# Kernel tuning notes

Measured on AMD Instinct MI355X. Metric: run time of the kernel, lower is better.

Reference implementation:

```python
import jax, jax.numpy as jnp
import numpy as np

B, L, D, H = 4, 1024, 1024, 16
DK = D // H


def setup_inputs() -> dict:
    key = jax.random.key(0)
    ks = jax.random.split(key, 5)
    s = 1.0 / np.sqrt(D)  # roughly nn.Linear init scale
    return {
        "x": jax.random.normal(ks[0], (B, L, D), dtype=jnp.float32),
        "Wq": jax.random.normal(ks[1], (D, D), dtype=jnp.float32) * s,
        "bq": jnp.zeros((D,), dtype=jnp.float32),
        "Wk": jax.random.normal(ks[2], (D, D), dtype=jnp.float32) * s,
        "bk": jnp.zeros((D,), dtype=jnp.float32),
        "Wv": jax.random.normal(ks[3], (D, D), dtype=jnp.float32) * s,
        "bv": jnp.zeros((D,), dtype=jnp.float32),
        "Wo": jax.random.normal(ks[4], (D, D), dtype=jnp.float32) * s,
        "bo": jnp.zeros((D,), dtype=jnp.float32),
    }


def reference(x, Wq, bq, Wk, bk, Wv, bv, Wo, bo):
    b, l, d = x.shape
    # torch Linear: y = x @ W.T + b
    q = (x @ Wq.T + bq).reshape(b, l, H, DK).transpose(0, 2, 1, 3)  # [B,H,L,DK]
    k = (x @ Wk.T + bk).reshape(b, l, H, DK).transpose(0, 2, 1, 3)
    v = (x @ Wv.T + bv).reshape(b, l, H, DK).transpose(0, 2, 1, 3)
    scores = jnp.einsum("bhqd,bhkd->bhqk", q, k) / jnp.sqrt(jnp.float32(DK))
    attn = jax.nn.softmax(scores, axis=-1)  # dropout p=0 -> identity
    head_out = jnp.einsum("bhqk,bhkd->bhqd", attn, v)  # [B,H,L,DK]
    merged = head_out.transpose(0, 2, 1, 3).reshape(b, l, d)  # [B,L,D]
    out = merged @ Wo.T + bo
    # DeCov loss over head outputs
    U = merged.reshape(b * l, d)
    U = U - U.mean(axis=0, keepdims=True)
    C = (U.T @ U) / jnp.float32(b * l)
    decov = 0.5 * (jnp.sum(C * C) - jnp.sum(jnp.diag(C) ** 2))
    return (out, decov)
```

## Files before the change

kernel.cpp:

```cpp
#include <hip/hip_runtime.h>
#include <cstdint>
#include <cstddef>

typedef short v4s __attribute__((ext_vector_type(4)));
typedef short v8s __attribute__((ext_vector_type(8)));
typedef float v4f __attribute__((ext_vector_type(4)));

__device__ __forceinline__ short f2bf(float f) {
    union { float f; unsigned u; } x; x.f = f;
    unsigned r = (x.u + 0x7FFFu + ((x.u >> 16) & 1u)) >> 16;
    return (short)(unsigned short)r;
}
__device__ __forceinline__ float bf2f(short h) {
    union { unsigned u; float f; } x; x.u = ((unsigned)(unsigned short)h) << 16;
    return x.f;
}

__device__ __forceinline__ void gld16(const void* g, void* l) {
    __builtin_amdgcn_global_load_lds((const __attribute__((address_space(1))) void*)g,
                                     (__attribute__((address_space(3))) void*)l, 16, 0, 0);
}

__global__ __launch_bounds__(256) void cvt_bf16(
    const float* __restrict__ x, const float* __restrict__ wq, const float* __restrict__ wk,
    const float* __restrict__ wv, const float* __restrict__ wo,
    short* __restrict__ xb, short* __restrict__ wqb, short* __restrict__ wkb,
    short* __restrict__ wvb, short* __restrict__ wob)
{
    int bid = blockIdx.x;
    const float* src; short* dst; size_t base;
    if (bid < 4096)      { src = x;  dst = xb;  base = (size_t)bid * 1024; }
    else if (bid < 5120) { src = wq; dst = wqb; base = (size_t)(bid - 4096) * 1024; }
    else if (bid < 6144) { src = wk; dst = wkb; base = (size_t)(bid - 5120) * 1024; }
    else if (bid < 7168) { src = wv; dst = wvb; base = (size_t)(bid - 6144) * 1024; }
    else                 { src = wo; dst = wob; base = (size_t)(bid - 7168) * 1024; }
    size_t idx = base + (size_t)threadIdx.x * 4;
    v4f v = *(const v4f*)(src + idx);
    v4s o;
    o[0] = f2bf(v[0]); o[1] = f2bf(v[1]); o[2] = f2bf(v[2]); o[3] = f2bf(v[3]);
    *(v4s*)(dst + idx) = o;
}

__global__ __launch_bounds__(256) void gemm_qkv(
    const short* __restrict__ xb,
    const short* __restrict__ wq, const short* __restrict__ wk, const short* __restrict__ wv,
    const float* __restrict__ bq, const float* __restrict__ bk, const float* __restrict__ bv,
    short* __restrict__ qo, short* __restrict__ ko, short* __restrict__ vto)
{
    __shared__ __align__(16) short At[128 * 32];
    __shared__ __align__(16) short Bt[128 * 32];
    const int K = 1024;
    const int mode = blockIdx.z;
    const short* W = (mode == 0) ? wq : (mode == 1) ? wk : wv;
    const float* bias = (mode == 0) ? bq : (mode == 1) ? bk : bv;
    const int m0 = blockIdx.y * 128, n0 = blockIdx.x * 128;
    const int tid = threadIdx.x, wave = tid >> 6, lane = tid & 63;
    const int quad = lane >> 4, ll = lane & 15;
    const int wr = wave >> 1, wc = wave & 1;
    const v4f zero4 = {0.f, 0.f, 0.f, 0.f};
    v4f acc[4][4];
    for (int i = 0; i < 4; ++i) for (int j = 0; j < 4; ++j) acc[i][j] = zero4;

    for (int k0 = 0; k0 < K; k0 += 32) {
        __syncthreads();
#pragma unroll
        for (int c = 0; c < 2; ++c) {
            int chb = (wave * 2 + c) * 64;
            int ch = chb + lane;
            int row = ch >> 2, col8 = (ch & 3) * 8;
            gld16(xb + (size_t)(m0 + row) * K + k0 + col8, &At[chb * 8]);
            gld16(W  + (size_t)(n0 + row) * K + k0 + col8, &Bt[chb * 8]);
        }
        __syncthreads();
        v8s af[4], bfr[4];
#pragma unroll
        for (int i = 0; i < 4; ++i) af[i]  = *(const v8s*)&At[(wr * 64 + i * 16 + ll) * 32 + quad * 8];
#pragma unroll
        for (int j = 0; j < 4; ++j) bfr[j] = *(const v8s*)&Bt[(wc * 64 + j * 16 + ll) * 32 + quad * 8];
#pragma unroll
        for (int i = 0; i < 4; ++i)
#pragma unroll
            for (int j = 0; j < 4; ++j)
                acc[i][j] = __builtin_amdgcn_mfma_f32_16x16x32_bf16(af[i], bfr[j], acc[i][j], 0, 0, 0);
    }

    const float scale = (mode == 0) ? 0.125f : 1.0f;
#pragma unroll
    for (int j = 0; j < 4; ++j) {
        int n = n0 + wc * 64 + j * 16 + ll;
        float bb = bias[n];
        int hh = n >> 6, dk = n & 63;
#pragma unroll
        for (int i = 0; i < 4; ++i) {
            int mbase = m0 + wr * 64 + i * 16 + quad * 4;
#pragma unroll
            for (int r = 0; r < 4; ++r) {
                int m = mbase + r;
                int b = m >> 10, li = m & 1023;
                short h = f2bf((acc[i][j][r] + bb) * scale);
                if (mode == 0)
                    qo[(((size_t)(b * 16 + hh) * 1024 + li) << 6) + dk] = h;
                else if (mode == 1)
                    ko[(((size_t)(b * 16 + hh) * 1024 + li) << 6) + dk] = h;
                else
                    vto[(((size_t)(b * 16 + hh) * 64 + dk) << 10) + li] = h;
            }
        }
    }
}

__global__ __launch_bounds__(256) void gemm_out(
    const short* __restrict__ A, const short* __restrict__ W,
    const float* __restrict__ bias, float* __restrict__ out)
{
    __shared__ __align__(16) short At[128 * 32];
    __shared__ __align__(16) short Bt[128 * 32];
    const int K = 1024;
    const int m0 = blockIdx.y * 128, n0 = blockIdx.x * 128;
    const int tid = threadIdx.x, wave = tid >> 6, lane = tid & 63;
    const int quad = lane >> 4, ll = lane & 15;
    const int wr = wave >> 1, wc = wave & 1;
    const v4f zero4 = {0.f, 0.f, 0.f, 0.f};
    v4f acc[4][4];
    for (int i = 0; i < 4; ++i) for (int j = 0; j < 4; ++j) acc[i][j] = zero4;

    for (int k0 = 0; k0 < K; k0 += 32) {
        __syncthreads();
#pragma unroll
        for (int c = 0; c < 2; ++c) {
            int chb = (wave * 2 + c) * 64;
            int ch = chb + lane;
            int row = ch >> 2, col8 = (ch & 3) * 8;
            gld16(A + (size_t)(m0 + row) * K + k0 + col8, &At[chb * 8]);
            gld16(W + (size_t)(n0 + row) * K + k0 + col8, &Bt[chb * 8]);
        }
        __syncthreads();
        v8s af[4], bfr[4];
#pragma unroll
        for (int i = 0; i < 4; ++i) af[i]  = *(const v8s*)&At[(wr * 64 + i * 16 + ll) * 32 + quad * 8];
#pragma unroll
        for (int j = 0; j < 4; ++j) bfr[j] = *(const v8s*)&Bt[(wc * 64 + j * 16 + ll) * 32 + quad * 8];
#pragma unroll
        for (int i = 0; i < 4; ++i)
#pragma unroll
            for (int j = 0; j < 4; ++j)
                acc[i][j] = __builtin_amdgcn_mfma_f32_16x16x32_bf16(af[i], bfr[j], acc[i][j], 0, 0, 0);
    }

#pragma unroll
    for (int j = 0; j < 4; ++j) {
        int n = n0 + wc * 64 + j * 16 + ll;
        float bb = bias[n];
#pragma unroll
        for (int i = 0; i < 4; ++i) {
            int mbase = m0 + wr * 64 + i * 16 + quad * 4;
#pragma unroll
            for (int r = 0; r < 4; ++r) {
                int m = mbase + r;
                out[(size_t)m * 1024 + n] = acc[i][j][r] + bb;
            }
        }
    }
}

__global__ __launch_bounds__(256) void attn_flash(
    const short* __restrict__ qb, const short* __restrict__ kb, const short* __restrict__ vtb,
    float* __restrict__ merged, short* __restrict__ mergedh)
{
    __shared__ __align__(16) short Kt[64 * 64];
    __shared__ __align__(16) short Vt[64 * 64];
    __shared__ __align__(16) short Pt[4 * 16 * 68];
    const int bh = blockIdx.y, qt = blockIdx.x;
    const int tid = threadIdx.x, wave = tid >> 6, lane = tid & 63;
    const int quad = lane >> 4, ll = lane & 15;
    const short* qp = qb  + (size_t)bh * 1024 * 64;
    const short* kp = kb  + (size_t)bh * 1024 * 64;
    const short* vp = vtb + (size_t)bh * 64 * 1024;

    const int qrow = qt * 64 + wave * 16 + ll;
    v8s qa0 = *(const v8s*)(qp + (size_t)qrow * 64 + quad * 8);
    v8s qa1 = *(const v8s*)(qp + (size_t)qrow * 64 + 32 + quad * 8);

    const v4f zero4 = {0.f, 0.f, 0.f, 0.f};
    v4f oacc[4];
    for (int nt = 0; nt < 4; ++nt) oacc[nt] = zero4;
    float lsum[4] = {0.f, 0.f, 0.f, 0.f};
    short* pw = &Pt[wave * 16 * 68];

    for (int jt = 0; jt < 16; ++jt) {
        __syncthreads();
#pragma unroll
        for (int c = 0; c < 2; ++c) {
            int chb = (wave * 2 + c) * 64;
            int ch = chb + lane;
            int row = ch >> 3;
            int gi = ((ch & 7) ^ (row & 7)) * 8;
            gld16(kp + (size_t)(jt * 64 + row) * 64 + gi, &Kt[chb * 8]);
            gld16(vp + (size_t)row * 1024 + jt * 64 + gi, &Vt[chb * 8]);
        }
        __syncthreads();

        v4f sacc[4];
#pragma unroll
        for (int nt = 0; nt < 4; ++nt) {
            int n = nt * 16 + ll;
            int g0 = (quad ^ (n & 7)) * 8;
            int g1 = ((4 + quad) ^ (n & 7)) * 8;
            v8s b0 = *(const v8s*)&Kt[n * 64 + g0];
            v8s b1 = *(const v8s*)&Kt[n * 64 + g1];
            v4f s = zero4;
            s = __builtin_amdgcn_mfma_f32_16x16x32_bf16(qa0, b0, s, 0, 0, 0);
            s = __builtin_amdgcn_mfma_f32_16x16x32_bf16(qa1, b1, s, 0, 0, 0);
            sacc[nt] = s;
        }
#pragma unroll
        for (int nt = 0; nt < 4; ++nt) {
#pragma unroll
            for (int r = 0; r < 4; ++r) {
                float e = __expf(sacc[nt][r]);
                lsum[r] += e;
                pw[(quad * 4 + r) * 68 + nt * 16 + ll] = f2bf(e);
            }
        }
        __syncthreads();
        v4s p00 = *(const v4s*)&pw[ll * 68 + quad * 8];
        v4s p01 = *(const v4s*)&pw[ll * 68 + quad * 8 + 4];
        v4s p10 = *(const v4s*)&pw[ll * 68 + 32 + quad * 8];
        v4s p11 = *(const v4s*)&pw[ll * 68 + 32 + quad * 8 + 4];
        v8s pa0 = __builtin_shufflevector(p00, p01, 0, 1, 2, 3, 4, 5, 6, 7);
        v8s pa1 = __builtin_shufflevector(p10, p11, 0, 1, 2, 3, 4, 5, 6, 7);
#pragma unroll
        for (int nt = 0; nt < 4; ++nt) {
            int n = nt * 16 + ll;
            int g0 = (quad ^ (n & 7)) * 8;
            int g1 = ((4 + quad) ^ (n & 7)) * 8;
            v8s v0 = *(const v8s*)&Vt[n * 64 + g0];
            v8s v1 = *(const v8s*)&Vt[n * 64 + g1];
            oacc[nt] = __builtin_amdgcn_mfma_f32_16x16x32_bf16(pa0, v0, oacc[nt], 0, 0, 0);
            oacc[nt] = __builtin_amdgcn_mfma_f32_16x16x32_bf16(pa1, v1, oacc[nt], 0, 0, 0);
        }
    }

    float linv[4];
#pragma unroll
    for (int r = 0; r < 4; ++r) {
        float s = lsum[r];
        s += __shfl_xor(s, 1); s += __shfl_xor(s, 2);
        s += __shfl_xor(s, 4); s += __shfl_xor(s, 8);
        linv[r] = 1.0f / s;
    }
    const int b = bh >> 4, h = bh & 15;
#pragma unroll
    for (int r = 0; r < 4; ++r) {
        int li = qt * 64 + wave * 16 + quad * 4 + r;
        size_t rowoff = ((size_t)(b * 1024 + li)) * 1024 + h * 64;
#pragma unroll
        for (int nt = 0; nt < 4; ++nt) {
            int d = nt * 16 + ll;
            float v = oacc[nt][r] * linv[r];
            merged[rowoff + d] = v;
            mergedh[rowoff + d] = f2bf(v);
        }
    }
}

__global__ __launch_bounds__(256) void col_part(const float* __restrict__ merged, float* __restrict__ part) {
    const int bi = blockIdx.x, t = threadIdx.x;
    const float* base = merged + (size_t)bi * 32 * 1024 + (size_t)t * 4;
    float s0 = 0.f, s1 = 0.f, s2 = 0.f, s3 = 0.f;
    for (int r = 0; r < 32; ++r) {
        v4f v = *(const v4f*)(base + (size_t)r * 1024);
        s0 += v[0]; s1 += v[1]; s2 += v[2]; s3 += v[3];
    }
    v4f o = {s0, s1, s2, s3};
    *(v4f*)(part + (size_t)bi * 1024 + (size_t)t * 4) = o;
}

__global__ __launch_bounds__(256) void col_mean(const float* __restrict__ part, float* __restrict__ mean) {
    int c = blockIdx.x * 256 + threadIdx.x;
    float s = 0.f;
    for (int i = 0; i < 128; ++i) s += part[i * 1024 + c];
    mean[c] = s * (1.0f / 4096.0f);
}

__global__ __launch_bounds__(256) void center_tr(
    const float* __restrict__ merged, const float* __restrict__ cmean,
    short* __restrict__ uth, short* __restrict__ utl)
{
    __shared__ short Hh[64][72];
    __shared__ short Hl[64][72];
    const int d0 = blockIdx.x * 64, m0 = blockIdx.y * 64;
    const int t = threadIdx.x;
    const int r0 = t >> 4, c4 = (t & 15) * 4;
    float mu[4];
#pragma unroll
    for (int e = 0; e < 4; ++e) mu[e] = cmean[d0 + c4 + e];
    for (int rr = 0; rr < 64; rr += 16) {
        int m = m0 + rr + r0;
        v4f v = *(const v4f*)(merged + (size_t)m * 1024 + d0 + c4);
#pragma unroll
        for (int e = 0; e < 4; ++e) {
            float u = v[e] - mu[e];
            short h = f2bf(u);
            Hh[c4 + e][rr + r0] = h;
            Hl[c4 + e][rr + r0] = f2bf(u - bf2f(h));
        }
    }
    __syncthreads();
    const int d = t >> 2, mg = (t & 3) * 16;
    v8s a0, a1, b0, b1;
#pragma unroll
    for (int e = 0; e < 8; ++e) {
        a0[e] = Hh[d][mg + e]; a1[e] = Hh[d][mg + 8 + e];
        b0[e] = Hl[d][mg + e]; b1[e] = Hl[d][mg + 8 + e];
    }
    size_t off = (size_t)(d0 + d) * 4096 + m0 + mg;
    *(v8s*)(uth + off) = a0; *(v8s*)(uth + off + 8) = a1;
    *(v8s*)(utl + off) = b0; *(v8s*)(utl + off + 8) = b1;
}

__global__ __launch_bounds__(256) void gemm_decov(
    const short* __restrict__ uth, const short* __restrict__ utl, float* __restrict__ cpart)
{
    int p = blockIdx.x, I = 0, rem = p;
    while (rem >= 16 - I) { rem -= 16 - I; ++I; }
    const int J = I + rem;
    const int kbase = blockIdx.y * 512;
    __shared__ __align__(16) short Ah[64 * 32], Al[64 * 32], Bh[64 * 32], Bl[64 * 32];
    const int tid = threadIdx.x;
    const int wave = tid >> 6, lane = tid & 63;
    const int quad = lane >> 4, ll = lane & 15;
    const int wr = wave >> 1, wc = wave & 1;
    const v4f zero4 = {0.f, 0.f, 0.f, 0.f};
    v4f acc[2][2];
    for (int i = 0; i < 2; ++i) for (int j = 0; j < 2; ++j) acc[i][j] = zero4;

    for (int kk = 0; kk < 512; kk += 32) {
        int k0 = kbase + kk;
        __syncthreads();
        {
            int ch = wave * 64 + lane;
            int row = ch >> 2, col8 = (ch & 3) * 8;
            gld16(uth + (size_t)(I * 64 + row) * 4096 + k0 + col8, &Ah[wave * 512]);
            gld16(utl + (size_t)(I * 64 + row) * 4096 + k0 + col8, &Al[wave * 512]);
            gld16(uth + (size_t)(J * 64 + row) * 4096 + k0 + col8, &Bh[wave * 512]);
            gld16(utl + (size_t)(J * 64 + row) * 4096 + k0 + col8, &Bl[wave * 512]);
        }
        __syncthreads();
        v8s ah[2], al[2], bh[2], bl[2];
#pragma unroll
        for (int i = 0; i < 2; ++i) {
            int ro = (wr * 32 + i * 16 + ll) * 32 + quad * 8;
            ah[i] = *(const v8s*)&Ah[ro];
            al[i] = *(const v8s*)&Al[ro];
        }
#pragma unroll
        for (int j = 0; j < 2; ++j) {
            int ro = (wc * 32 + j * 16 + ll) * 32 + quad * 8;
            bh[j] = *(const v8s*)&Bh[ro];
            bl[j] = *(const v8s*)&Bl[ro];
        }
#pragma unroll
        for (int i = 0; i < 2; ++i)
#pragma unroll
            for (int j = 0; j < 2; ++j) {
                acc[i][j] = __builtin_amdgcn_mfma_f32_16x16x32_bf16(ah[i], bh[j], acc[i][j], 0, 0, 0);
                acc[i][j] = __builtin_amdgcn_mfma_f32_16x16x32_bf16(ah[i], bl[j], acc[i][j], 0, 0, 0);
                acc[i][j] = __builtin_amdgcn_mfma_f32_16x16x32_bf16(al[i], bh[j], acc[i][j], 0, 0, 0);
            }
    }

    float* dst = cpart + ((size_t)blockIdx.y * 136 + p) * 4096;
#pragma unroll
    for (int i = 0; i < 2; ++i)
#pragma unroll
        for (int j = 0; j < 2; ++j)
#pragma unroll
            for (int r = 0; r < 4; ++r) {
                int gi2 = wr * 32 + i * 16 + quad * 4 + r;
                int gj2 = wc * 32 + j * 16 + ll;
                dst[gi2 * 64 + gj2] = acc[i][j][r];
            }
}

__global__ __launch_bounds__(256) void decov_reduce(const float* __restrict__ cpart, float* __restrict__ dsum) {
    int p = blockIdx.x, I = 0, rem = p;
    while (rem >= 16 - I) { rem -= 16 - I; ++I; }
    const int J = I + rem;
    const int t = threadIdx.x;
    __shared__ float wsums[4];
    float s = 0.f;
    for (int e = t; e < 4096; e += 256) {
        float c = 0.f;
#pragma unroll
        for (int kc = 0; kc < 8; ++kc) c += cpart[((size_t)kc * 136 + p) * 4096 + e];
        int gi = I * 64 + (e >> 6), gj = J * 64 + (e & 63);
        if (gi != gj) s += c * c;
    }
    if (I < J) s *= 2.f;
    s += __shfl_xor(s, 1); s += __shfl_xor(s, 2); s += __shfl_xor(s, 4);
    s += __shfl_xor(s, 8); s += __shfl_xor(s, 16); s += __shfl_xor(s, 32);
    if ((t & 63) == 0) wsums[t >> 6] = s;
    __syncthreads();
    if (t == 0) dsum[p] = wsums[0] + wsums[1] + wsums[2] + wsums[3];
}

__global__ __launch_bounds__(256) void decov_final(const float* __restrict__ dsum, float* __restrict__ out) {
    const int t = threadIdx.x;
    __shared__ float wsums[4];
    float s = (t < 136) ? dsum[t] : 0.f;
    s += __shfl_xor(s, 1); s += __shfl_xor(s, 2); s += __shfl_xor(s, 4);
    s += __shfl_xor(s, 8); s += __shfl_xor(s, 16); s += __shfl_xor(s, 32);
    if ((t & 63) == 0) wsums[t >> 6] = s;
    __syncthreads();
    if (t == 0) {
        float tot = wsums[0] + wsums[1] + wsums[2] + wsums[3];
        out[4194304] = 0.5f * tot / (4096.0f * 4096.0f);
    }
}

extern "C" void kernel_launch(void* const* d_in, const int* in_sizes, int n_in,
                              void* d_out, int out_size, void* d_ws, size_t ws_size,
                              hipStream_t stream) {
    const float* x  = (const float*)d_in[0];
    const float* Wq = (const float*)d_in[1];
    const float* bq = (const float*)d_in[2];
    const float* Wk = (const float*)d_in[3];
    const float* bk = (const float*)d_in[4];
    const float* Wv = (const float*)d_in[5];
    const float* bv = (const float*)d_in[6];
    const float* Wo = (const float*)d_in[7];
    const float* bo = (const float*)d_in[8];
    float* out = (float*)d_out;
    char* ws = (char*)d_ws;
    const size_t MB = 1ull << 20;
    short* xb      = (short*)(ws);
    short* wqb     = (short*)(ws + 8  * MB);
    short* wkb     = (short*)(ws + 10 * MB);
    short* wvb     = (short*)(ws + 12 * MB);
    short* wob     = (short*)(ws + 14 * MB);
    short* qb      = (short*)(ws + 16 * MB);
    short* kb      = (short*)(ws + 24 * MB);
    short* vtb     = (short*)(ws + 32 * MB);
    float* merged  = (float*)(ws + 40 * MB);
    short* mergedh = (short*)(ws + 56 * MB);
    float* colpart = (float*)(ws + 64 * MB);
    float* colmean = (float*)(ws + 64 * MB + 512 * 1024);
    short* uth     = (short*)(ws + 65 * MB);
    short* utl     = (short*)(ws + 73 * MB);
    float* dsum    = (float*)(ws + 81 * MB);
    float* cpart   = (float*)(ws);

    hipLaunchKernelGGL(cvt_bf16, dim3(8192), dim3(256), 0, stream,
                       x, Wq, Wk, Wv, Wo, xb, wqb, wkb, wvb, wob);
    hipLaunchKernelGGL(gemm_qkv, dim3(8, 32, 3), dim3(256), 0, stream,
                       xb, wqb, wkb, wvb, bq, bk, bv, qb, kb, vtb);
    hipLaunchKernelGGL(attn_flash, dim3(16, 64), dim3(256), 0, stream,
                       qb, kb, vtb, merged, mergedh);
    hipLaunchKernelGGL(gemm_out, dim3(8, 32), dim3(256), 0, stream,
                       mergedh, wob, bo, out);
    hipLaunchKernelGGL(col_part, dim3(128), dim3(256), 0, stream, merged, colpart);
    hipLaunchKernelGGL(col_mean, dim3(4), dim3(256), 0, stream, colpart, colmean);
    hipLaunchKernelGGL(center_tr, dim3(16, 64), dim3(256), 0, stream,
                       merged, colmean, uth, utl);
    hipLaunchKernelGGL(gemm_decov, dim3(136, 8), dim3(256), 0, stream, uth, utl, cpart);
    hipLaunchKernelGGL(decov_reduce, dim3(136), dim3(256), 0, stream, cpart, dsum);
    hipLaunchKernelGGL(decov_final, dim3(1), dim3(256), 0, stream, dsum, out);
}
```

Before: 252.3 us.

## Double GEMM K-tile with XOR-swizzled LDS and give attention waves 32 query rows

The three MFMA GEMM kernels (QKV projection, output projection, DeCov covariance) now stage 64-wide K tiles instead of 32. They use an XOR-swizzled LDS layout, which halves the number of barriers per K and is meant to avoid bank conflicts on the fragment reads. The flash attention kernel now gives each wave 32 query rows instead of 16 and launches half as many blocks. Each K/V tile loaded into LDS is therefore reused across twice as many queries. The trade-off is higher register and LDS use, fewer blocks, and lower occupancy.

```diff
diff --git a/kernel.cpp b/kernel.cpp
--- a/kernel.cpp
+++ b/kernel.cpp
@@ -47,8 +47,8 @@
     const float* __restrict__ bq, const float* __restrict__ bk, const float* __restrict__ bv,
     short* __restrict__ qo, short* __restrict__ ko, short* __restrict__ vto)
 {
-    __shared__ __align__(16) short At[128 * 32];
-    __shared__ __align__(16) short Bt[128 * 32];
+    __shared__ __align__(16) short At[128 * 64];
+    __shared__ __align__(16) short Bt[128 * 64];
     const int K = 1024;
     const int mode = blockIdx.z;
     const short* W = (mode == 0) ? wq : (mode == 1) ? wk : wv;
@@ -61,27 +61,33 @@
     v4f acc[4][4];
     for (int i = 0; i < 4; ++i) for (int j = 0; j < 4; ++j) acc[i][j] = zero4;
 
-    for (int k0 = 0; k0 < K; k0 += 32) {
-        __syncthreads();
-#pragma unroll
-        for (int c = 0; c < 2; ++c) {
-            int chb = (wave * 2 + c) * 64;
-            int ch = chb + lane;
-            int row = ch >> 2, col8 = (ch & 3) * 8;
-            gld16(xb + (size_t)(m0 + row) * K + k0 + col8, &At[chb * 8]);
-            gld16(W  + (size_t)(n0 + row) * K + k0 + col8, &Bt[chb * 8]);
-        }
-        __syncthreads();
-        v8s af[4], bfr[4];
-#pragma unroll
-        for (int i = 0; i < 4; ++i) af[i]  = *(const v8s*)&At[(wr * 64 + i * 16 + ll) * 32 + quad * 8];
-#pragma unroll
-        for (int j = 0; j < 4; ++j) bfr[j] = *(const v8s*)&Bt[(wc * 64 + j * 16 + ll) * 32 + quad * 8];
-#pragma unroll
-        for (int i = 0; i < 4; ++i)
-#pragma unroll
-            for (int j = 0; j < 4; ++j)
-                acc[i][j] = __builtin_amdgcn_mfma_f32_16x16x32_bf16(af[i], bfr[j], acc[i][j], 0, 0, 0);
+    const int srow = (lane >> 3);
+    const int sgi = ((lane & 7) ^ srow) * 8;
+
+    for (int k0 = 0; k0 < K; k0 += 64) {
+        __syncthreads();
+#pragma unroll
+        for (int c = 0; c < 4; ++c) {
+            int g = wave * 4 + c;
+            int row = g * 8 + srow;
+            gld16(xb + (size_t)(m0 + row) * K + k0 + sgi, &At[g * 512]);
+            gld16(W  + (size_t)(n0 + row) * K + k0 + sgi, &Bt[g * 512]);
+        }
+        __syncthreads();
+#pragma unroll
+        for (int s = 0; s < 2; ++s) {
+            const int xo = ((s * 4 + quad) ^ (ll & 7)) * 8;
+            v8s af[4], bfr[4];
+#pragma unroll
+            for (int i = 0; i < 4; ++i) af[i]  = *(const v8s*)&At[(wr * 64 + i * 16 + ll) * 64 + xo];
+#pragma unroll
+            for (int j = 0; j < 4; ++j) bfr[j] = *(const v8s*)&Bt[(wc * 64 + j * 16 + ll) * 64 + xo];
+#pragma unroll
+            for (int i = 0; i < 4; ++i)
+#pragma unroll
+                for (int j = 0; j < 4; ++j)
+                    acc[i][j] = __builtin_amdgcn_mfma_f32_16x16x32_bf16(af[i], bfr[j], acc[i][j], 0, 0, 0);
+        }
     }
 
     const float scale = (mode == 0) ? 0.125f : 1.0f;
@@ -113,8 +119,8 @@
     const short* __restrict__ A, const short* __restrict__ W,
     const float* __restrict__ bias, float* __restrict__ out)
 {
-    __shared__ __align__(16) short At[128 * 32];
-    __shared__ __align__(16) short Bt[128 * 32];
+    __shared__ __align__(16) short At[128 * 64];
+    __shared__ __align__(16) short Bt[128 * 64];
     const int K = 1024;
     const int m0 = blockIdx.y * 128, n0 = blockIdx.x * 128;
     const int tid = threadIdx.x, wave = tid >> 6, lane = tid & 63;
@@ -124,27 +130,33 @@
     v4f acc[4][4];
     for (int i = 0; i < 4; ++i) for (int j = 0; j < 4; ++j) acc[i][j] = zero4;
 
-    for (int k0 = 0; k0 < K; k0 += 32) {
-        __syncthreads();
-#pragma unroll
-        for (int c = 0; c < 2; ++c) {
-            int chb = (wave * 2 + c) * 64;
-            int ch = chb + lane;
-            int row = ch >> 2, col8 = (ch & 3) * 8;
-            gld16(A + (size_t)(m0 + row) * K + k0 + col8, &At[chb * 8]);
-            gld16(W + (size_t)(n0 + row) * K + k0 + col8, &Bt[chb * 8]);
-        }
-        __syncthreads();
-        v8s af[4], bfr[4];
-#pragma unroll
-        for (int i = 0; i < 4; ++i) af[i]  = *(const v8s*)&At[(wr * 64 + i * 16 + ll) * 32 + quad * 8];
-#pragma unroll
-        for (int j = 0; j < 4; ++j) bfr[j] = *(const v8s*)&Bt[(wc * 64 + j * 16 + ll) * 32 + quad * 8];
-#pragma unroll
-        for (int i = 0; i < 4; ++i)
-#pragma unroll
-            for (int j = 0; j < 4; ++j)
-                acc[i][j] = __builtin_amdgcn_mfma_f32_16x16x32_bf16(af[i], bfr[j], acc[i][j], 0, 0, 0);
+    const int srow = (lane >> 3);
+    const int sgi = ((lane & 7) ^ srow) * 8;
+
+    for (int k0 = 0; k0 < K; k0 += 64) {
+        __syncthreads();
+#pragma unroll
+        for (int c = 0; c < 4; ++c) {
+            int g = wave * 4 + c;
+            int row = g * 8 + srow;
+            gld16(A + (size_t)(m0 + row) * K + k0 + sgi, &At[g * 512]);
+            gld16(W + (size_t)(n0 + row) * K + k0 + sgi, &Bt[g * 512]);
+        }
+        __syncthreads();
+#pragma unroll
+        for (int s = 0; s < 2; ++s) {
+            const int xo = ((s * 4 + quad) ^ (ll & 7)) * 8;
+            v8s af[4], bfr[4];
+#pragma unroll
+            for (int i = 0; i < 4; ++i) af[i]  = *(const v8s*)&At[(wr * 64 + i * 16 + ll) * 64 + xo];
+#pragma unroll
+            for (int j = 0; j < 4; ++j) bfr[j] = *(const v8s*)&Bt[(wc * 64 + j * 16 + ll) * 64 + xo];
+#pragma unroll
+            for (int i = 0; i < 4; ++i)
+#pragma unroll
+                for (int j = 0; j < 4; ++j)
+                    acc[i][j] = __builtin_amdgcn_mfma_f32_16x16x32_bf16(af[i], bfr[j], acc[i][j], 0, 0, 0);
+        }
     }
 
 #pragma unroll
@@ -169,7 +181,7 @@
 {
     __shared__ __align__(16) short Kt[64 * 64];
     __shared__ __align__(16) short Vt[64 * 64];
-    __shared__ __align__(16) short Pt[4 * 16 * 68];
+    __shared__ __align__(16) short Pt[4 * 32 * 68];
     const int bh = blockIdx.y, qt = blockIdx.x;
     const int tid = threadIdx.x, wave = tid >> 6, lane = tid & 63;
     const int quad = lane >> 4, ll = lane & 15;
@@ -177,15 +189,20 @@
     const short* kp = kb  + (size_t)bh * 1024 * 64;
     const short* vp = vtb + (size_t)bh * 64 * 1024;
 
-    const int qrow = qt * 64 + wave * 16 + ll;
-    v8s qa0 = *(const v8s*)(qp + (size_t)qrow * 64 + quad * 8);
-    v8s qa1 = *(const v8s*)(qp + (size_t)qrow * 64 + 32 + quad * 8);
+    v8s qa[2][2];
+#pragma unroll
+    for (int mi = 0; mi < 2; ++mi) {
+        int qrow = qt * 128 + wave * 32 + mi * 16 + ll;
+        qa[mi][0] = *(const v8s*)(qp + (size_t)qrow * 64 + quad * 8);
+        qa[mi][1] = *(const v8s*)(qp + (size_t)qrow * 64 + 32 + quad * 8);
+    }
 
     const v4f zero4 = {0.f, 0.f, 0.f, 0.f};
-    v4f oacc[4];
-    for (int nt = 0; nt < 4; ++nt) oacc[nt] = zero4;
-    float lsum[4] = {0.f, 0.f, 0.f, 0.f};
-    short* pw = &Pt[wave * 16 * 68];
+    v4f oacc[2][4];
+    for (int mi = 0; mi < 2; ++mi) for (int nt = 0; nt < 4; ++nt) oacc[mi][nt] = zero4;
+    float lsum[2][4];
+    for (int mi = 0; mi < 2; ++mi) for (int r = 0; r < 4; ++r) lsum[mi][r] = 0.f;
+    short* pw = &Pt[wave * 32 * 68];
 
     for (int jt = 0; jt < 16; ++jt) {
         __syncthreads();
@@ -200,7 +217,7 @@
         }
         __syncthreads();
 
-        v4f sacc[4];
+        v4f sacc[2][4];
 #pragma unroll
         for (int nt = 0; nt < 4; ++nt) {
             int n = nt * 16 + ll;
@@ -208,27 +225,35 @@
             int g1 = ((4 + quad) ^ (n & 7)) * 8;
             v8s b0 = *(const v8s*)&Kt[n * 64 + g0];
             v8s b1 = *(const v8s*)&Kt[n * 64 + g1];
-            v4f s = zero4;
-            s = __builtin_amdgcn_mfma_f32_16x16x32_bf16(qa0, b0, s, 0, 0, 0);
-            s = __builtin_amdgcn_mfma_f32_16x16x32_bf16(qa1, b1, s, 0, 0, 0);
-            sacc[nt] = s;
-        }
-#pragma unroll
-        for (int nt = 0; nt < 4; ++nt) {
-#pragma unroll
-            for (int r = 0; r < 4; ++r) {
-                float e = __expf(sacc[nt][r]);
-                lsum[r] += e;
-                pw[(quad * 4 + r) * 68 + nt * 16 + ll] = f2bf(e);
-            }
-        }
-        __syncthreads();
-        v4s p00 = *(const v4s*)&pw[ll * 68 + quad * 8];
-        v4s p01 = *(const v4s*)&pw[ll * 68 + quad * 8 + 4];
-        v4s p10 = *(const v4s*)&pw[ll * 68 + 32 + quad * 8];
-        v4s p11 = *(const v4s*)&pw[ll * 68 + 32 + quad * 8 + 4];
-        v8s pa0 = __builtin_shufflevector(p00, p01, 0, 1, 2, 3, 4, 5, 6, 7);
-        v8s pa1 = __builtin_shufflevector(p10, p11, 0, 1, 2, 3, 4, 5, 6, 7);
+#pragma unroll
+            for (int mi = 0; mi < 2; ++mi) {
+                v4f s = zero4;
+                s = __builtin_amdgcn_mfma_f32_16x16x32_bf16(qa[mi][0], b0, s, 0, 0, 0);
+                s = __builtin_amdgcn_mfma_f32_16x16x32_bf16(qa[mi][1], b1, s, 0, 0, 0);
+                sacc[mi][nt] = s;
+            }
+        }
+#pragma unroll
+        for (int mi = 0; mi < 2; ++mi)
+#pragma unroll
+            for (int nt = 0; nt < 4; ++nt)
+#pragma unroll
+                for (int r = 0; r < 4; ++r) {
+                    float e = __expf(sacc[mi][nt][r]);
+                    lsum[mi][r] += e;
+                    pw[(mi * 16 + quad * 4 + r) * 68 + nt * 16 + ll] = f2bf(e);
+                }
+        __syncthreads();
+        v8s pa[2][2];
+#pragma unroll
+        for (int mi = 0; mi < 2; ++mi) {
+            v4s p00 = *(const v4s*)&pw[(mi * 16 + ll) * 68 + quad * 8];
+            v4s p01 = *(const v4s*)&pw[(mi * 16 + ll) * 68 + quad * 8 + 4];
+            v4s p10 = *(const v4s*)&pw[(mi * 16 + ll) * 68 + 32 + quad * 8];
+            v4s p11 = *(const v4s*)&pw[(mi * 16 + ll) * 68 + 32 + quad * 8 + 4];
+            pa[mi][0] = __builtin_shufflevector(p00, p01, 0, 1, 2, 3, 4, 5, 6, 7);
+            pa[mi][1] = __builtin_shufflevector(p10, p11, 0, 1, 2, 3, 4, 5, 6, 7);
+        }
 #pragma unroll
         for (int nt = 0; nt < 4; ++nt) {
             int n = nt * 16 + ll;
@@ -236,30 +261,36 @@
             int g1 = ((4 + quad) ^ (n & 7)) * 8;
             v8s v0 = *(const v8s*)&Vt[n * 64 + g0];
             v8s v1 = *(const v8s*)&Vt[n * 64 + g1];
-            oacc[nt] = __builtin_amdgcn_mfma_f32_16x16x32_bf16(pa0, v0, oacc[nt], 0, 0, 0);
-            oacc[nt] = __builtin_amdgcn_mfma_f32_16x16x32_bf16(pa1, v1, oacc[nt], 0, 0, 0);
-        }
-    }
-
-    float linv[4];
-#pragma unroll
-    for (int r = 0; r < 4; ++r) {
-        float s = lsum[r];
-        s += __shfl_xor(s, 1); s += __shfl_xor(s, 2);
-        s += __shfl_xor(s, 4); s += __shfl_xor(s, 8);
-        linv[r] = 1.0f / s;
-    }
+#pragma unroll
+            for (int mi = 0; mi < 2; ++mi) {
+                oacc[mi][nt] = __builtin_amdgcn_mfma_f32_16x16x32_bf16(pa[mi][0], v0, oacc[mi][nt], 0, 0, 0);
+                oacc[mi][nt] = __builtin_amdgcn_mfma_f32_16x16x32_bf16(pa[mi][1], v1, oacc[mi][nt], 0, 0, 0);
+            }
+        }
+    }
+
     const int b = bh >> 4, h = bh & 15;
 #pragma unroll
-    for (int r = 0; r < 4; ++r) {
-        int li = qt * 64 + wave * 16 + quad * 4 + r;
-        size_t rowoff = ((size_t)(b * 1024 + li)) * 1024 + h * 64;
-#pragma unroll
-        for (int nt = 0; nt < 4; ++nt) {
-            int d = nt * 16 + ll;
-            float v = oacc[nt][r] * linv[r];
-            merged[rowoff + d] = v;
-            mergedh[rowoff + d] = f2bf(v);
+    for (int mi = 0; mi < 2; ++mi) {
+        float linv[4];
+#pragma unroll
+        for (int r = 0; r < 4; ++r) {
+            float s = lsum[mi][r];
+            s += __shfl_xor(s, 1); s += __shfl_xor(s, 2);
+            s += __shfl_xor(s, 4); s += __shfl_xor(s, 8);
+            linv[r] = 1.0f / s;
+        }
+#pragma unroll
+        for (int r = 0; r < 4; ++r) {
+            int li = qt * 128 + wave * 32 + mi * 16 + quad * 4 + r;
+            size_t rowoff = ((size_t)(b * 1024 + li)) * 1024 + h * 64;
+#pragma unroll
+            for (int nt = 0; nt < 4; ++nt) {
+                int d = nt * 16 + ll;
+                float v = oacc[mi][nt][r] * linv[r];
+                merged[rowoff + d] = v;
+                mergedh[rowoff + d] = f2bf(v);
+            }
         }
     }
 }
@@ -326,7 +357,7 @@
     while (rem >= 16 - I) { rem -= 16 - I; ++I; }
     const int J = I + rem;
     const int kbase = blockIdx.y * 512;
-    __shared__ __align__(16) short Ah[64 * 32], Al[64 * 32], Bh[64 * 32], Bl[64 * 32];
+    __shared__ __align__(16) short Ah[64 * 64], Al[64 * 64], Bh[64 * 64], Bl[64 * 64];
     const int tid = threadIdx.x;
     const int wave = tid >> 6, lane = tid & 63;
     const int quad = lane >> 4, ll = lane & 15;
@@ -335,39 +366,47 @@
     v4f acc[2][2];
     for (int i = 0; i < 2; ++i) for (int j = 0; j < 2; ++j) acc[i][j] = zero4;
 
-    for (int kk = 0; kk < 512; kk += 32) {
+    const int srow = (lane >> 3);
+    const int sgi = ((lane & 7) ^ srow) * 8;
+
+    for (int kk = 0; kk < 512; kk += 64) {
         int k0 = kbase + kk;
         __syncthreads();
-        {
-            int ch = wave * 64 + lane;
-            int row = ch >> 2, col8 = (ch & 3) * 8;
-            gld16(uth + (size_t)(I * 64 + row) * 4096 + k0 + col8, &Ah[wave * 512]);
-            gld16(utl + (size_t)(I * 64 + row) * 4096 + k0 + col8, &Al[wave * 512]);
-            gld16(uth + (size_t)(J * 64 + row) * 4096 + k0 + col8, &Bh[wave * 512]);
-            gld16(utl + (size_t)(J * 64 + row) * 4096 + k0 + col8, &Bl[wave * 512]);
-        }
-        __syncthreads();
-        v8s ah[2], al[2], bh[2], bl[2];
-#pragma unroll
-        for (int i = 0; i < 2; ++i) {
-            int ro = (wr * 32 + i * 16 + ll) * 32 + quad * 8;
-            ah[i] = *(const v8s*)&Ah[ro];
-            al[i] = *(const v8s*)&Al[ro];
-        }
-#pragma unroll
-        for (int j = 0; j < 2; ++j) {
-            int ro = (wc * 32 + j * 16 + ll) * 32 + quad * 8;
-            bh[j] = *(const v8s*)&Bh[ro];
-            bl[j] = *(const v8s*)&Bl[ro];
-        }
-#pragma unroll
-        for (int i = 0; i < 2; ++i)
+#pragma unroll
+        for (int c = 0; c < 2; ++c) {
+            int g = wave * 2 + c;
+            int row = g * 8 + srow;
+            gld16(uth + (size_t)(I * 64 + row) * 4096 + k0 + sgi, &Ah[g * 512]);
+            gld16(utl + (size_t)(I * 64 + row) * 4096 + k0 + sgi, &Al[g * 512]);
+            gld16(uth + (size_t)(J * 64 + row) * 4096 + k0 + sgi, &Bh[g * 512]);
+            gld16(utl + (size_t)(J * 64 + row) * 4096 + k0 + sgi, &Bl[g * 512]);
+        }
+        __syncthreads();
+#pragma unroll
+        for (int s = 0; s < 2; ++s) {
+            const int xo = ((s * 4 + quad) ^ (ll & 7)) * 8;
+            v8s ah[2], al[2], bh[2], bl[2];
+#pragma unroll
+            for (int i = 0; i < 2; ++i) {
+                int ro = (wr * 32 + i * 16 + ll) * 64 + xo;
+                ah[i] = *(const v8s*)&Ah[ro];
+                al[i] = *(const v8s*)&Al[ro];
+            }
 #pragma unroll
             for (int j = 0; j < 2; ++j) {
-                acc[i][j] = __builtin_amdgcn_mfma_f32_16x16x32_bf16(ah[i], bh[j], acc[i][j], 0, 0, 0);
-                acc[i][j] = __builtin_amdgcn_mfma_f32_16x16x32_bf16(ah[i], bl[j], acc[i][j], 0, 0, 0);
-                acc[i][j] = __builtin_amdgcn_mfma_f32_16x16x32_bf16(al[i], bh[j], acc[i][j], 0, 0, 0);
-            }
+                int ro = (wc * 32 + j * 16 + ll) * 64 + xo;
+                bh[j] = *(const v8s*)&Bh[ro];
+                bl[j] = *(const v8s*)&Bl[ro];
+            }
+#pragma unroll
+            for (int i = 0; i < 2; ++i)
+#pragma unroll
+                for (int j = 0; j < 2; ++j) {
+                    acc[i][j] = __builtin_amdgcn_mfma_f32_16x16x32_bf16(ah[i], bh[j], acc[i][j], 0, 0, 0);
+                    acc[i][j] = __builtin_amdgcn_mfma_f32_16x16x32_bf16(ah[i], bl[j], acc[i][j], 0, 0, 0);
+                    acc[i][j] = __builtin_amdgcn_mfma_f32_16x16x32_bf16(al[i], bh[j], acc[i][j], 0, 0, 0);
+                }
+        }
     }
 
     float* dst = cpart + ((size_t)blockIdx.y * 136 + p) * 4096;
@@ -455,7 +494,7 @@
                        x, Wq, Wk, Wv, Wo, xb, wqb, wkb, wvb, wob);
     hipLaunchKernelGGL(gemm_qkv, dim3(8, 32, 3), dim3(256), 0, stream,
                        xb, wqb, wkb, wvb, bq, bk, bv, qb, kb, vtb);
-    hipLaunchKernelGGL(attn_flash, dim3(16, 64), dim3(256), 0, stream,
+    hipLaunchKernelGGL(attn_flash, dim3(8, 64), dim3(256), 0, stream,
                        qb, kb, vtb, merged, mergedh);
     hipLaunchKernelGGL(gemm_out, dim3(8, 32), dim3(256), 0, stream,
                        mergedh, wob, bo, out);
```

Result: slower. 265.4 us (+5.2%).

## Fuse column-sum into attention and decov reductions into GEMM via atomic counters

Applied to the files above, without the earlier changes.

Column sums of the merged head outputs are now accumulated in the attention epilogue with atomicAdd, which removes the separate col_part and col_mean kernels and their re-read of merged. The decov_reduce and decov_final kernels are folded into gemm_decov using last-block-done counters: the last K-split block for each pair reduces its tile, and the last pair block produces the scalar. This cuts four launches and a full pass over merged, at the cost of a memset, atomics, threadfences and a float summation order that is no longer deterministic.

```diff
diff --git a/kernel.cpp b/kernel.cpp
--- a/kernel.cpp
+++ b/kernel.cpp
@@ -165,7 +165,7 @@
 
 __global__ __launch_bounds__(256) void attn_flash(
     const short* __restrict__ qb, const short* __restrict__ kb, const short* __restrict__ vtb,
-    float* __restrict__ merged, short* __restrict__ mergedh)
+    float* __restrict__ merged, short* __restrict__ mergedh, float* __restrict__ colsum)
 {
     __shared__ __align__(16) short Kt[64 * 64];
     __shared__ __align__(16) short Vt[64 * 64];
@@ -250,6 +250,7 @@
         linv[r] = 1.0f / s;
     }
     const int b = bh >> 4, h = bh & 15;
+    float csum[4] = {0.f, 0.f, 0.f, 0.f};
 #pragma unroll
     for (int r = 0; r < 4; ++r) {
         int li = qt * 64 + wave * 16 + quad * 4 + r;
@@ -260,31 +261,23 @@
             float v = oacc[nt][r] * linv[r];
             merged[rowoff + d] = v;
             mergedh[rowoff + d] = f2bf(v);
-        }
-    }
-}
-
-__global__ __launch_bounds__(256) void col_part(const float* __restrict__ merged, float* __restrict__ part) {
-    const int bi = blockIdx.x, t = threadIdx.x;
-    const float* base = merged + (size_t)bi * 32 * 1024 + (size_t)t * 4;
-    float s0 = 0.f, s1 = 0.f, s2 = 0.f, s3 = 0.f;
-    for (int r = 0; r < 32; ++r) {
-        v4f v = *(const v4f*)(base + (size_t)r * 1024);
-        s0 += v[0]; s1 += v[1]; s2 += v[2]; s3 += v[3];
-    }
-    v4f o = {s0, s1, s2, s3};
-    *(v4f*)(part + (size_t)bi * 1024 + (size_t)t * 4) = o;
-}
-
-__global__ __launch_bounds__(256) void col_mean(const float* __restrict__ part, float* __restrict__ mean) {
-    int c = blockIdx.x * 256 + threadIdx.x;
-    float s = 0.f;
-    for (int i = 0; i < 128; ++i) s += part[i * 1024 + c];
-    mean[c] = s * (1.0f / 4096.0f);
+            csum[nt] += v;
+        }
+    }
+#pragma unroll
+    for (int nt = 0; nt < 4; ++nt) {
+        csum[nt] += __shfl_xor(csum[nt], 16);
+        csum[nt] += __shfl_xor(csum[nt], 32);
+    }
+    if (quad == 0) {
+#pragma unroll
+        for (int nt = 0; nt < 4; ++nt)
+            atomicAdd(&colsum[h * 64 + nt * 16 + ll], csum[nt]);
+    }
 }
 
 __global__ __launch_bounds__(256) void center_tr(
-    const float* __restrict__ merged, const float* __restrict__ cmean,
+    const float* __restrict__ merged, const float* __restrict__ colsum,
     short* __restrict__ uth, short* __restrict__ utl)
 {
     __shared__ short Hh[64][72];
@@ -294,7 +287,7 @@
     const int r0 = t >> 4, c4 = (t & 15) * 4;
     float mu[4];
 #pragma unroll
-    for (int e = 0; e < 4; ++e) mu[e] = cmean[d0 + c4 + e];
+    for (int e = 0; e < 4; ++e) mu[e] = colsum[d0 + c4 + e] * (1.0f / 4096.0f);
     for (int rr = 0; rr < 64; rr += 16) {
         int m = m0 + rr + r0;
         v4f v = *(const v4f*)(merged + (size_t)m * 1024 + d0 + c4);
@@ -320,13 +313,17 @@
 }
 
 __global__ __launch_bounds__(256) void gemm_decov(
-    const short* __restrict__ uth, const short* __restrict__ utl, float* __restrict__ cpart)
+    const short* __restrict__ uth, const short* __restrict__ utl, float* __restrict__ cpart,
+    float* __restrict__ dsum, int* __restrict__ paircnt, int* __restrict__ gcnt,
+    float* __restrict__ out)
 {
     int p = blockIdx.x, I = 0, rem = p;
     while (rem >= 16 - I) { rem -= 16 - I; ++I; }
     const int J = I + rem;
     const int kbase = blockIdx.y * 512;
     __shared__ __align__(16) short Ah[64 * 32], Al[64 * 32], Bh[64 * 32], Bl[64 * 32];
+    __shared__ float wsums[4];
+    __shared__ int sflag;
     const int tid = threadIdx.x;
     const int wave = tid >> 6, lane = tid & 63;
     const int quad = lane >> 4, ll = lane & 15;
@@ -381,16 +378,15 @@
                 int gj2 = wc * 32 + j * 16 + ll;
                 dst[gi2 * 64 + gj2] = acc[i][j][r];
             }
-}
-
-__global__ __launch_bounds__(256) void decov_reduce(const float* __restrict__ cpart, float* __restrict__ dsum) {
-    int p = blockIdx.x, I = 0, rem = p;
-    while (rem >= 16 - I) { rem -= 16 - I; ++I; }
-    const int J = I + rem;
-    const int t = threadIdx.x;
-    __shared__ float wsums[4];
+
+    __threadfence();
+    if (tid == 0) sflag = atomicAdd(&paircnt[p], 1);
+    __syncthreads();
+    if (sflag != 7) return;
+    __threadfence();
+
     float s = 0.f;
-    for (int e = t; e < 4096; e += 256) {
+    for (int e = tid; e < 4096; e += 256) {
         float c = 0.f;
 #pragma unroll
         for (int kc = 0; kc < 8; ++kc) c += cpart[((size_t)kc * 136 + p) * 4096 + e];
@@ -400,20 +396,23 @@
     if (I < J) s *= 2.f;
     s += __shfl_xor(s, 1); s += __shfl_xor(s, 2); s += __shfl_xor(s, 4);
     s += __shfl_xor(s, 8); s += __shfl_xor(s, 16); s += __shfl_xor(s, 32);
-    if ((t & 63) == 0) wsums[t >> 6] = s;
+    if (lane == 0) wsums[wave] = s;
     __syncthreads();
-    if (t == 0) dsum[p] = wsums[0] + wsums[1] + wsums[2] + wsums[3];
-}
-
-__global__ __launch_bounds__(256) void decov_final(const float* __restrict__ dsum, float* __restrict__ out) {
-    const int t = threadIdx.x;
-    __shared__ float wsums[4];
-    float s = (t < 136) ? dsum[t] : 0.f;
-    s += __shfl_xor(s, 1); s += __shfl_xor(s, 2); s += __shfl_xor(s, 4);
-    s += __shfl_xor(s, 8); s += __shfl_xor(s, 16); s += __shfl_xor(s, 32);
-    if ((t & 63) == 0) wsums[t >> 6] = s;
+    if (tid == 0) {
+        dsum[p] = wsums[0] + wsums[1] + wsums[2] + wsums[3];
+        __threadfence();
+        sflag = atomicAdd(gcnt, 1);
+    }
     __syncthreads();
-    if (t == 0) {
+    if (sflag != 135) return;
+    __threadfence();
+
+    float t2 = (tid < 136) ? dsum[tid] : 0.f;
+    t2 += __shfl_xor(t2, 1); t2 += __shfl_xor(t2, 2); t2 += __shfl_xor(t2, 4);
+    t2 += __shfl_xor(t2, 8); t2 += __shfl_xor(t2, 16); t2 += __shfl_xor(t2, 32);
+    if (lane == 0) wsums[wave] = t2;
+    __syncthreads();
+    if (tid == 0) {
         float tot = wsums[0] + wsums[1] + wsums[2] + wsums[3];
         out[4194304] = 0.5f * tot / (4096.0f * 4096.0f);
     }
@@ -444,26 +443,26 @@
     short* vtb     = (short*)(ws + 32 * MB);
     float* merged  = (float*)(ws + 40 * MB);
     short* mergedh = (short*)(ws + 56 * MB);
-    float* colpart = (float*)(ws + 64 * MB);
-    float* colmean = (float*)(ws + 64 * MB + 512 * 1024);
     short* uth     = (short*)(ws + 65 * MB);
     short* utl     = (short*)(ws + 73 * MB);
-    float* dsum    = (float*)(ws + 81 * MB);
+    char*  ctrl    = ws + 81 * MB;
+    float* dsum    = (float*)(ctrl);
+    int*   paircnt = (int*)(ctrl + 1024);
+    int*   gcnt    = (int*)(ctrl + 1568);
+    float* colsum  = (float*)(ctrl + 4096);
     float* cpart   = (float*)(ws);
 
+    hipMemsetAsync(ctrl, 0, 8192, stream);
     hipLaunchKernelGGL(cvt_bf16, dim3(8192), dim3(256), 0, stream,
                        x, Wq, Wk, Wv, Wo, xb, wqb, wkb, wvb, wob);
     hipLaunchKernelGGL(gemm_qkv, dim3(8, 32, 3), dim3(256), 0, stream,
                        xb, wqb, wkb, wvb, bq, bk, bv, qb, kb, vtb);
     hipLaunchKernelGGL(attn_flash, dim3(16, 64), dim3(256), 0, stream,
-                       qb, kb, vtb, merged, mergedh);
+                       qb, kb, vtb, merged, mergedh, colsum);
     hipLaunchKernelGGL(gemm_out, dim3(8, 32), dim3(256), 0, stream,
                        mergedh, wob, bo, out);
-    hipLaunchKernelGGL(col_part, dim3(128), dim3(256), 0, stream, merged, colpart);
-    hipLaunchKernelGGL(col_mean, dim3(4), dim3(256), 0, stream, colpart, colmean);
     hipLaunchKernelGGL(center_tr, dim3(16, 64), dim3(256), 0, stream,
-                       merged, colmean, uth, utl);
-    hipLaunchKernelGGL(gemm_decov, dim3(136, 8), dim3(256), 0, stream, uth, utl, cpart);
-    hipLaunchKernelGGL(decov_reduce, dim3(136), dim3(256), 0, stream, cpart, dsum);
-    hipLaunchKernelGGL(decov_final, dim3(1), dim3(256), 0, stream, dsum, out);
-}
+                       merged, colsum, uth, utl);
+    hipLaunchKernelGGL(gemm_decov, dim3(136, 8), dim3(256), 0, stream,
+                       uth, utl, cpart, dsum, paircnt, gcnt, out);
+}
```

Measured after the change: 400.9 us. 58.9% more time.
